# Kernel optimization log

Hardware: AMD Instinct MI355X
Metric: run time of the kernel (lower is better)

The kernel has to match this reference:

```python
import jax, jax.numpy as jnp
import numpy as np

B, S, I, H, E, V = 32, 128, 1024, 1024, 1024, 32000


def setup_inputs() -> dict:
    key = jax.random.key(0)
    ks = jax.random.split(key, 16)
    s = 0.02
    return {
        "x": jax.random.normal(ks[0], (1, B, I), jnp.float32),
        "encoder_outputs": jax.random.normal(ks[1], (S, B, E), jnp.float32),
        "hidden": jax.random.normal(ks[2], (1, B, H), jnp.float32),
        # GRU params (torch layout: gates r, z, n stacked)
        "W_ih": jax.random.normal(ks[3], (3 * H, I), jnp.float32) * s,
        "W_hh": jax.random.normal(ks[4], (3 * H, H), jnp.float32) * s,
        "b_ih": jnp.zeros((3 * H,), jnp.float32),
        "b_hh": jnp.zeros((3 * H,), jnp.float32),
        # attn: Linear(hidden + enc_hidden -> hidden)
        "W_attn": jax.random.normal(ks[5], (H, H + E), jnp.float32) * s,
        "b_attn": jnp.zeros((H,), jnp.float32),
        # attn_combine: Linear(input + enc_hidden -> input)
        "W_comb": jax.random.normal(ks[6], (I, I + E), jnp.float32) * s,
        "b_comb": jnp.zeros((I,), jnp.float32),
        # out: Linear(hidden -> vocab)
        "W_out": jax.random.normal(ks[7], (V, H), jnp.float32) * s,
        "b_out": jnp.zeros((V,), jnp.float32),
    }


def reference(x, encoder_outputs, hidden,
              W_ih, W_hh, b_ih, b_hh,
              W_attn, b_attn, W_comb, b_comb, W_out, b_out):
    Hd = hidden.shape[-1]
    x0, h0 = x[0], hidden[0]                     # [B,I], [B,H]
    # --- single GRU step (torch gate order r, z, n) ---
    xg = x0 @ W_ih.T + b_ih                      # [B,3H]
    hg = h0 @ W_hh.T + b_hh                      # [B,3H]
    r = jax.nn.sigmoid(xg[:, :Hd] + hg[:, :Hd])
    z = jax.nn.sigmoid(xg[:, Hd:2 * Hd] + hg[:, Hd:2 * Hd])
    n = jnp.tanh(xg[:, 2 * Hd:] + r * hg[:, 2 * Hd:])
    dec = (1.0 - z) * n + z * h0                 # [B,H] decoder_output
    # --- batched Bahdanau-style score: dec_b . attn([dec_b; enc_sb]) ---
    Sn = encoder_outputs.shape[0]
    dec_rep = jnp.broadcast_to(dec[None], (Sn,) + dec.shape)      # [S,B,H]
    cat = jnp.concatenate([dec_rep, encoder_outputs], axis=-1)    # [S,B,H+E]
    proj = jnp.einsum('sbc,hc->sbh', cat, W_attn) + b_attn        # [S,B,H]
    scores = jnp.einsum('bh,sbh->bs', dec, proj)                  # [B,S]
    attn_weights = jax.nn.softmax(scores, axis=-1)                # [B,S]
    context = jnp.einsum('bs,sbe->be', attn_weights, encoder_outputs)  # [B,E]
    # --- combine input + context, project to vocab, log-softmax ---
    comb = jnp.concatenate([x0, context], axis=-1) @ W_comb.T + b_comb  # [B,I]
    output = jax.nn.log_softmax(comb @ W_out.T + b_out, axis=-1)        # [B,V]
    return output, attn_weights
```

## Files before the change

### kernel.cpp

```cpp
#include <hip/hip_runtime.h>
#include <hip/hip_bf16.h>
#include <math.h>

#define BDIM 32
#define HD   1024
#define SD   128
#define VD   32000

typedef __attribute__((ext_vector_type(8))) short short8;
typedef __attribute__((ext_vector_type(4))) float floatx4;

__device__ __forceinline__ short f2bf(float f) {
    unsigned u = __builtin_bit_cast(unsigned, f);
    u += 0x7FFFu + ((u >> 16) & 1u);
    return (short)(u >> 16);
}
__device__ __forceinline__ float bf2f(short h) {
    unsigned u = ((unsigned)(unsigned short)h) << 16;
    return __builtin_bit_cast(float, u);
}
__device__ __forceinline__ unsigned pack2(float a, float b) {
    unsigned ua = __builtin_bit_cast(unsigned, a) + 0x8000u;
    unsigned ub = __builtin_bit_cast(unsigned, b) + 0x8000u;
    return (ub & 0xffff0000u) | (ua >> 16);
}

__device__ __forceinline__ int swz_idx(int b, int k) {
    int t = k >> 5, q = (k & 31) >> 3, j = k & 7;
    int mt = b >> 4, i = b & 15;
    return ((((t * 2 + mt) * 64) + q * 16 + i) << 3) + j;
}

#define MFMA(a, b, c) __builtin_amdgcn_mfma_f32_16x16x32_bf16(a, b, c, 0, 0, 0)

__global__ __launch_bounds__(256) void prep_swz(
    const float* __restrict__ x0, const float* __restrict__ h0,
    short* __restrict__ x0h, short* __restrict__ x0l,
    short* __restrict__ h0h, short* __restrict__ h0l)
{
    int idx = blockIdx.x * 256 + threadIdx.x;
    if (idx < 32768) {
        int b = idx >> 10, k = idx & 1023;
        float xv = x0[idx]; short hh = f2bf(xv);
        int d = swz_idx(b, k);
        x0h[d] = hh; x0l[d] = f2bf(xv - bf2f(hh));
    } else {
        idx -= 32768;
        int b = idx >> 10, k = idx & 1023;
        float xv = h0[idx]; short hh = f2bf(xv);
        int d = swz_idx(b, k);
        h0h[d] = hh; h0l[d] = f2bf(xv - bf2f(hh));
    }
}

template<int KCHUNK>
__device__ __forceinline__ void gemm_gates_body(
    const short* __restrict__ bhi, const short* __restrict__ blo,
    const float* __restrict__ W, float* __restrict__ out, int N, int K, int k0)
{
    int tid = threadIdx.x;
    int w = tid >> 6, l = tid & 63;
    int i = l & 15, q = l >> 4;
    int n0 = blockIdx.x * 64 + w * 16;
    const float* wrow = W + (size_t)(n0 + i) * K + q * 8;
    const short8* bph = (const short8*)bhi + l;
    const short8* bpl = (const short8*)blo + l;

    floatx4 acc0 = {0.f, 0.f, 0.f, 0.f};
    floatx4 acc1 = {0.f, 0.f, 0.f, 0.f};

#pragma unroll 2
    for (int kk = k0; kk < k0 + KCHUNK; kk += 32) {
        float4 w0 = *(const float4*)(wrow + kk);
        float4 w1 = *(const float4*)(wrow + kk + 4);
        float wf[8] = {w0.x, w0.y, w0.z, w0.w, w1.x, w1.y, w1.z, w1.w};
        short8 ahi, alo;
#pragma unroll
        for (int j = 0; j < 8; ++j) {
            short hh = f2bf(wf[j]);
            ahi[j] = hh;
            alo[j] = f2bf(wf[j] - bf2f(hh));
        }
        int t2 = (kk >> 5) * 2;
        short8 b0 = bph[(size_t)t2 * 64];
        short8 b1 = bph[(size_t)(t2 + 1) * 64];
        short8 l0 = bpl[(size_t)t2 * 64];
        short8 l1 = bpl[(size_t)(t2 + 1) * 64];
        acc0 = MFMA(ahi, b0, acc0);
        acc1 = MFMA(ahi, b1, acc1);
        acc0 = MFMA(ahi, l0, acc0);
        acc1 = MFMA(ahi, l1, acc1);
        acc0 = MFMA(alo, b0, acc0);
        acc1 = MFMA(alo, b1, acc1);
    }

    __shared__ float lds[4][32][17];
#pragma unroll
    for (int r = 0; r < 4; ++r) {
        lds[w][i][q * 4 + r]      = acc0[r];
        lds[w][i + 16][q * 4 + r] = acc1[r];
    }
    __syncthreads();
    int b = l >> 1, hf = l & 1;
    size_t obase = (size_t)b * N + n0 + hf * 8;
#pragma unroll
    for (int t = 0; t < 8; ++t) atomicAdd(out + obase + t, lds[w][b][hf * 8 + t]);
}

__global__ __launch_bounds__(256) void gemm_gates(
    const short* __restrict__ x0h, const short* __restrict__ x0l,
    const short* __restrict__ h0h, const short* __restrict__ h0l,
    const float* __restrict__ W_ih, const float* __restrict__ W_hh,
    float* __restrict__ xg, float* __restrict__ hg)
{
    if (blockIdx.z == 0)
        gemm_gates_body<512>(x0h, x0l, W_ih, xg, 3072, 1024, blockIdx.y * 512);
    else
        gemm_gates_body<512>(h0h, h0l, W_hh, hg, 3072, 1024, blockIdx.y * 512);
}

__global__ __launch_bounds__(256) void gru_gate(
    const float* __restrict__ xg, const float* __restrict__ hg,
    const float* __restrict__ h0,
    const float* __restrict__ b_ih, const float* __restrict__ b_hh,
    short* __restrict__ dh, short* __restrict__ dl)
{
    int idx = blockIdx.x * 256 + threadIdx.x;
    int b = idx >> 10, h = idx & 1023;
    const float* xp = xg + (size_t)b * 3072 + h;
    const float* hp = hg + (size_t)b * 3072 + h;
    float r = 1.f / (1.f + __expf(-(xp[0] + b_ih[h] + hp[0] + b_hh[h])));
    float z = 1.f / (1.f + __expf(-(xp[1024] + b_ih[1024 + h] +
                                    hp[1024] + b_hh[1024 + h])));
    float n = tanhf(xp[2048] + b_ih[2048 + h] + r * (hp[2048] + b_hh[2048 + h]));
    float dec = (1.f - z) * n + z * h0[idx];
    short hh = f2bf(dec);
    int d = swz_idx(b, h);
    dh[d] = hh; dl[d] = f2bf(dec - bf2f(hh));
}

__global__ __launch_bounds__(256) void gemm_attn2(
    const short* __restrict__ dhi, const short* __restrict__ dlo,
    const float* __restrict__ Wa, float* __restrict__ v)
{
    int tid = threadIdx.x, w = tid >> 6, l = tid & 63;
    int i = l & 15, q = l >> 4;
    int e0 = blockIdx.x * 64;
    int k0 = blockIdx.y * 128;
    __shared__ float lds[32][65];

    const short8* ah = (const short8*)dhi;
    const short8* al = (const short8*)dlo;
    short8 Ah[4][2], Al[4][2];
#pragma unroll
    for (int t = 0; t < 4; ++t)
#pragma unroll
        for (int mt = 0; mt < 2; ++mt) {
            size_t idx = (size_t)((((k0 >> 5) + t) * 2 + mt) * 64) + l;
            Ah[t][mt] = ah[idx]; Al[t][mt] = al[idx];
        }

    floatx4 acc[2] = {{0.f,0.f,0.f,0.f},{0.f,0.f,0.f,0.f}};
    int sr = tid >> 3;
    int sc_ = (tid & 7) * 8;
#pragma unroll
    for (int t = 0; t < 4; ++t) {
        const float* src = Wa + (size_t)(k0 + t * 32 + sr) * 2048 + 1024 + e0 + sc_;
        float4 s0 = *(const float4*)src;
        float4 s1 = *(const float4*)(src + 4);
        __syncthreads();
        *(float4*)&lds[sr][sc_]     = s0;
        *(float4*)&lds[sr][sc_ + 4] = s1;
        __syncthreads();
        short8 Bh, Bl;
#pragma unroll
        for (int j = 0; j < 8; ++j) {
            float f = lds[q * 8 + j][w * 16 + i];
            unsigned u = __builtin_bit_cast(unsigned, f);
            float hif = __builtin_bit_cast(float, u & 0xffff0000u);
            Bh[j] = (short)(u >> 16);
            float lo = f - hif;
            Bl[j] = (short)(__builtin_bit_cast(unsigned, lo) >> 16);
        }
        acc[0] = MFMA(Ah[t][0], Bh, acc[0]);
        acc[1] = MFMA(Ah[t][1], Bh, acc[1]);
        acc[0] = MFMA(Ah[t][0], Bl, acc[0]);
        acc[1] = MFMA(Ah[t][1], Bl, acc[1]);
        acc[0] = MFMA(Al[t][0], Bh, acc[0]);
        acc[1] = MFMA(Al[t][1], Bh, acc[1]);
    }
#pragma unroll
    for (int mt = 0; mt < 2; ++mt)
#pragma unroll
        for (int r = 0; r < 4; ++r)
            atomicAdd(v + (size_t)(mt * 16 + q * 4 + r) * 1024 + e0 + w * 16 + i,
                      acc[mt][r]);
}

__global__ __launch_bounds__(256) void scores_ctx(
    const float* __restrict__ v, const float* __restrict__ enc,
    float* __restrict__ num, float* __restrict__ den, float* __restrict__ es)
{
    int b = blockIdx.y, tid = threadIdx.x;
    int s0 = blockIdx.x * 8;
    int w = tid >> 6, l = tid & 63;
    float4 vv = *((const float4*)(v + (size_t)b * 1024) + tid);
    float4 e8[8];
    float part[8];
#pragma unroll
    for (int s = 0; s < 8; ++s) {
        float4 e4 = *((const float4*)(enc + ((size_t)(s0 + s) * BDIM + b) * 1024) + tid);
        e8[s] = e4;
        part[s] = e4.x * vv.x + e4.y * vv.y + e4.z * vv.z + e4.w * vv.w;
    }
    __shared__ float red[4][8];
    __shared__ float esl[8];
#pragma unroll
    for (int s = 0; s < 8; ++s) {
        float p = part[s];
        for (int o = 32; o; o >>= 1) p += __shfl_down(p, o);
        if (l == 0) red[w][s] = p;
    }
    __syncthreads();
    if (tid < 8) {
        float sc = red[0][tid] + red[1][tid] + red[2][tid] + red[3][tid];
        float e = __expf(sc);
        esl[tid] = e;
        es[b * SD + s0 + tid] = e;
    }
    __syncthreads();
    if (tid == 0) {
        float ds = 0.f;
#pragma unroll
        for (int s = 0; s < 8; ++s) ds += esl[s];
        atomicAdd(den + b, ds);
    }
    float n0 = 0.f, n1 = 0.f, n2 = 0.f, n3 = 0.f;
#pragma unroll
    for (int s = 0; s < 8; ++s) {
        float e = esl[s];
        n0 += e * e8[s].x; n1 += e * e8[s].y;
        n2 += e * e8[s].z; n3 += e * e8[s].w;
    }
    float* np = num + (size_t)b * 1024 + tid * 4;
    atomicAdd(np, n0); atomicAdd(np + 1, n1);
    atomicAdd(np + 2, n2); atomicAdd(np + 3, n3);
}

__global__ __launch_bounds__(256) void gemm_comb2(
    const float* __restrict__ x0, const float* __restrict__ num,
    const float* __restrict__ den, const float* __restrict__ es,
    const float* __restrict__ W_comb, float* __restrict__ comb,
    float* __restrict__ aw_out)
{
    int tid = threadIdx.x;
    int w = tid >> 6, l = tid & 63;
    int i = l & 15, q = l >> 4;
    int n0 = blockIdx.x * 64 + w * 16;
    int k0 = blockIdx.y * 256;
    __shared__ short cfrag[8192];

    if (blockIdx.x == 0) {
        int base = blockIdx.y * 512 + tid * 2;
#pragma unroll
        for (int j = 0; j < 2; ++j) {
            int idx = base + j;
            aw_out[idx] = es[idx] / den[idx >> 7];
        }
    }
    for (int ii = tid; ii < 8192; ii += 256) {
        int b = ii >> 8, kl = ii & 255;
        int k = k0 + kl;
        float xv = (k < 1024) ? x0[(b << 10) + k]
                              : num[(b << 10) + (k & 1023)] / den[b];
        cfrag[swz_idx(b, kl)] = f2bf(xv);
    }
    __syncthreads();

    const float* wrow = W_comb + (size_t)(n0 + i) * 2048 + k0 + q * 8;
    const short8* bp = (const short8*)cfrag + l;
    floatx4 acc0 = {0.f, 0.f, 0.f, 0.f};
    floatx4 acc1 = {0.f, 0.f, 0.f, 0.f};
#pragma unroll 2
    for (int kl = 0; kl < 256; kl += 32) {
        float4 w0 = *(const float4*)(wrow + kl);
        float4 w1 = *(const float4*)(wrow + kl + 4);
        union { unsigned u[4]; short8 s; } pk;
        pk.u[0] = pack2(w0.x, w0.y);
        pk.u[1] = pack2(w0.z, w0.w);
        pk.u[2] = pack2(w1.x, w1.y);
        pk.u[3] = pack2(w1.z, w1.w);
        int t2 = (kl >> 5) * 2;
        short8 b0 = bp[t2 * 64];
        short8 b1 = bp[(t2 + 1) * 64];
        acc0 = MFMA(pk.s, b0, acc0);
        acc1 = MFMA(pk.s, b1, acc1);
    }
    __shared__ float lds[4][32][17];
#pragma unroll
    for (int r = 0; r < 4; ++r) {
        lds[w][i][q * 4 + r]      = acc0[r];
        lds[w][i + 16][q * 4 + r] = acc1[r];
    }
    __syncthreads();
    int b = l >> 1, hf = l & 1;
    size_t obase = (size_t)b * 1024 + n0 + hf * 8;
#pragma unroll
    for (int t = 0; t < 8; ++t) atomicAdd(comb + obase + t, lds[w][b][hf * 8 + t]);
}

__global__ __launch_bounds__(256) void gemm_out2(
    const float* __restrict__ comb, const float* __restrict__ b_comb,
    const float* __restrict__ W, const float* __restrict__ bias,
    float* __restrict__ out, float* __restrict__ sexp)
{
    int tid = threadIdx.x, w = tid >> 6, l = tid & 63;
    int i = l & 15, q = l >> 4;
    int n0 = blockIdx.x * 64 + w * 16;
    __shared__ short cfrag[32768];
    __shared__ float lds[4][32][17];
    __shared__ float bsum[32];
    if (tid < 32) bsum[tid] = 0.f;
    for (int ii = tid; ii < 32768; ii += 256) {
        int b = ii >> 10, k = ii & 1023;
        cfrag[swz_idx(b, k)] = f2bf(comb[ii] + b_comb[k]);
    }
    __syncthreads();

    const float* wrow = W + (size_t)(n0 + i) * 1024 + q * 8;
    const short8* bp = (const short8*)cfrag + l;
    floatx4 acc0 = {0.f, 0.f, 0.f, 0.f};
    floatx4 acc1 = {0.f, 0.f, 0.f, 0.f};
#pragma unroll 4
    for (int kk = 0; kk < 1024; kk += 32) {
        float4 w0 = *(const float4*)(wrow + kk);
        float4 w1 = *(const float4*)(wrow + kk + 4);
        union { unsigned u[4]; short8 s; } pk;
        pk.u[0] = pack2(w0.x, w0.y);
        pk.u[1] = pack2(w0.z, w0.w);
        pk.u[2] = pack2(w1.x, w1.y);
        pk.u[3] = pack2(w1.z, w1.w);
        int t2 = (kk >> 5) * 2;
        short8 b0 = bp[t2 * 64];
        short8 b1 = bp[(t2 + 1) * 64];
        acc0 = MFMA(pk.s, b0, acc0);
        acc1 = MFMA(pk.s, b1, acc1);
    }
#pragma unroll
    for (int r = 0; r < 4; ++r) {
        lds[w][i][q * 4 + r]      = acc0[r];
        lds[w][i + 16][q * 4 + r] = acc1[r];
    }
    __syncthreads();
    int b = l >> 1, hf = l & 1;
    float vo[8];
#pragma unroll
    for (int t = 0; t < 8; ++t) vo[t] = lds[w][b][hf * 8 + t];
    const float4* bp4 = (const float4*)(bias + n0 + hf * 8);
    float4 bb0 = bp4[0], bb1 = bp4[1];
    vo[0] += bb0.x; vo[1] += bb0.y; vo[2] += bb0.z; vo[3] += bb0.w;
    vo[4] += bb1.x; vo[5] += bb1.y; vo[6] += bb1.z; vo[7] += bb1.w;
    float esum = 0.f;
#pragma unroll
    for (int t = 0; t < 8; ++t) esum += __expf(vo[t]);
    atomicAdd(&bsum[b], esum);
    float4 o0 = {vo[0], vo[1], vo[2], vo[3]};
    float4 o1 = {vo[4], vo[5], vo[6], vo[7]};
    float4* op = (float4*)(out + (size_t)b * VD + n0 + hf * 8);
    op[0] = o0; op[1] = o1;
    __syncthreads();
    if (tid < 32) atomicAdd(sexp + tid, bsum[tid]);
}

__global__ __launch_bounds__(256) void final_k(
    float* __restrict__ out, const float* __restrict__ sexp)
{
    int b = blockIdx.y;
    int vv = blockIdx.x * 256 + threadIdx.x;
    size_t o = (size_t)b * VD + vv;
    out[o] -= logf(sexp[b]);
}

extern "C" void kernel_launch(void* const* d_in, const int* in_sizes, int n_in,
                              void* d_out, int out_size, void* d_ws, size_t ws_size,
                              hipStream_t stream) {
    const float* x      = (const float*)d_in[0];
    const float* enc    = (const float*)d_in[1];
    const float* hid    = (const float*)d_in[2];
    const float* W_ih   = (const float*)d_in[3];
    const float* W_hh   = (const float*)d_in[4];
    const float* b_ih   = (const float*)d_in[5];
    const float* b_hh   = (const float*)d_in[6];
    const float* W_attn = (const float*)d_in[7];
    const float* W_comb = (const float*)d_in[9];
    const float* b_comb = (const float*)d_in[10];
    const float* W_out  = (const float*)d_in[11];
    const float* b_out  = (const float*)d_in[12];
    float* out = (float*)d_out;

    float* wsf  = (float*)d_ws;
    float* xg   = wsf;
    float* hg   = xg + 98304;
    float* v    = hg + 98304;
    float* num  = v + 32768;
    float* den  = num + 32768;
    float* sexp = den + 32;
    float* comb = sexp + 32;
    size_t zcount = 98304u * 2 + 32768u * 3 + 64;
    float* es   = comb + 32768;
    short* x0h  = (short*)(es + 4096);
    short* x0l  = x0h + 32768;
    short* h0h  = x0l + 32768;
    short* h0l  = h0h + 32768;
    short* dh   = h0l + 32768;
    short* dl   = dh + 32768;

    hipMemsetAsync(wsf, 0, zcount * sizeof(float), stream);
    prep_swz<<<256, 256, 0, stream>>>(x, hid, x0h, x0l, h0h, h0l);
    gemm_gates<<<dim3(48, 2, 2), 256, 0, stream>>>(
        x0h, x0l, h0h, h0l, W_ih, W_hh, xg, hg);
    gru_gate<<<128, 256, 0, stream>>>(xg, hg, hid, b_ih, b_hh, dh, dl);
    gemm_attn2<<<dim3(16, 8), 256, 0, stream>>>(dh, dl, W_attn, v);
    scores_ctx<<<dim3(16, 32), 256, 0, stream>>>(v, enc, num, den, es);
    gemm_comb2<<<dim3(16, 8), 256, 0, stream>>>(
        x, num, den, es, W_comb, comb, out + 1024000);
    gemm_out2<<<500, 256, 0, stream>>>(comb, b_comb, W_out, b_out, out, sexp);
    final_k<<<dim3(125, 32), 256, 0, stream>>>(out, sexp);
}
```

Measured before the change: 347.7 us.

## Fuse all decoder stages into one persistent kernel with grid barriers

Replaces the chain of eight kernel launches plus a large memset with a single persistent kernel of 512 blocks. Stages are separated by atomic-counter grid barriers, and zeroing of the workspace moves inside the kernel. The separate swizzle prep pass is dropped: the gate and combine GEMMs now read and split the activations directly. The output GEMM gets register double-buffered weight loads and one wave per 16-column tile. This removes launch gaps and intermediate traffic, but relies on all 512 blocks being co-resident (launch_bounds 256,2) and adds grid-barrier spin cost.

Result: slower. 655.2 us (+88.4%).

```diff
diff --git a/kernel.cpp b/kernel.cpp
--- a/kernel.cpp
+++ b/kernel.cpp
@@ -2,10 +2,7 @@
 #include <hip/hip_bf16.h>
 #include <math.h>
 
-#define BDIM 32
-#define HD   1024
-#define SD   128
-#define VD   32000
+#define VD 32000
 
 typedef __attribute__((ext_vector_type(8))) short short8;
 typedef __attribute__((ext_vector_type(4))) float floatx4;
@@ -24,361 +21,356 @@
     unsigned ub = __builtin_bit_cast(unsigned, b) + 0x8000u;
     return (ub & 0xffff0000u) | (ua >> 16);
 }
-
-__device__ __forceinline__ int swz_idx(int b, int k) {
-    int t = k >> 5, q = (k & 31) >> 3, j = k & 7;
-    int mt = b >> 4, i = b & 15;
-    return ((((t * 2 + mt) * 64) + q * 16 + i) << 3) + j;
+__device__ __forceinline__ void split8(const float4 u0, const float4 u1,
+                                       short8* hi, short8* lo) {
+    float f[8] = {u0.x, u0.y, u0.z, u0.w, u1.x, u1.y, u1.z, u1.w};
+#pragma unroll
+    for (int j = 0; j < 8; ++j) {
+        short h = f2bf(f[j]);
+        (*hi)[j] = h;
+        (*lo)[j] = f2bf(f[j] - bf2f(h));
+    }
+}
+__device__ __forceinline__ short8 pack8(const float4 u0, const float4 u1) {
+    union { unsigned u[4]; short8 s; } pk;
+    pk.u[0] = pack2(u0.x, u0.y); pk.u[1] = pack2(u0.z, u0.w);
+    pk.u[2] = pack2(u1.x, u1.y); pk.u[3] = pack2(u1.z, u1.w);
+    return pk.s;
 }
 
 #define MFMA(a, b, c) __builtin_amdgcn_mfma_f32_16x16x32_bf16(a, b, c, 0, 0, 0)
 
-__global__ __launch_bounds__(256) void prep_swz(
-    const float* __restrict__ x0, const float* __restrict__ h0,
-    short* __restrict__ x0h, short* __restrict__ x0l,
-    short* __restrict__ h0h, short* __restrict__ h0l)
+__device__ __forceinline__ void gbar(unsigned* bar, int ph, unsigned nb) {
+    __syncthreads();
+    if (threadIdx.x == 0) {
+        __threadfence();
+        __atomic_fetch_add(bar + ph, 1u, __ATOMIC_RELAXED);
+        while (__atomic_load_n(bar + ph, __ATOMIC_RELAXED) < nb)
+            __builtin_amdgcn_s_sleep(2);
+        __threadfence();
+    }
+    __syncthreads();
+}
+
+
+__global__ __launch_bounds__(256, 2) void mega(
+    const float* __restrict__ x0, const float* __restrict__ enc,
+    const float* __restrict__ h0,
+    const float* __restrict__ W_ih, const float* __restrict__ W_hh,
+    const float* __restrict__ b_ih, const float* __restrict__ b_hh,
+    const float* __restrict__ W_attn, const float* __restrict__ W_comb,
+    const float* __restrict__ b_comb, const float* __restrict__ W_out,
+    const float* __restrict__ b_out, float* __restrict__ out,
+    float* __restrict__ ws)
 {
-    int idx = blockIdx.x * 256 + threadIdx.x;
-    if (idx < 32768) {
-        int b = idx >> 10, k = idx & 1023;
-        float xv = x0[idx]; short hh = f2bf(xv);
-        int d = swz_idx(b, k);
-        x0h[d] = hh; x0l[d] = f2bf(xv - bf2f(hh));
-    } else {
-        idx -= 32768;
-        int b = idx >> 10, k = idx & 1023;
-        float xv = h0[idx]; short hh = f2bf(xv);
-        int d = swz_idx(b, k);
-        h0h[d] = hh; h0l[d] = f2bf(xv - bf2f(hh));
-    }
-}
-
-template<int KCHUNK>
-__device__ __forceinline__ void gemm_gates_body(
-    const short* __restrict__ bhi, const short* __restrict__ blo,
-    const float* __restrict__ W, float* __restrict__ out, int N, int K, int k0)
-{
-    int tid = threadIdx.x;
-    int w = tid >> 6, l = tid & 63;
-    int i = l & 15, q = l >> 4;
-    int n0 = blockIdx.x * 64 + w * 16;
-    const float* wrow = W + (size_t)(n0 + i) * K + q * 8;
-    const short8* bph = (const short8*)bhi + l;
-    const short8* bpl = (const short8*)blo + l;
-
-    floatx4 acc0 = {0.f, 0.f, 0.f, 0.f};
-    floatx4 acc1 = {0.f, 0.f, 0.f, 0.f};
-
-#pragma unroll 2
-    for (int kk = k0; kk < k0 + KCHUNK; kk += 32) {
-        float4 w0 = *(const float4*)(wrow + kk);
-        float4 w1 = *(const float4*)(wrow + kk + 4);
-        float wf[8] = {w0.x, w0.y, w0.z, w0.w, w1.x, w1.y, w1.z, w1.w};
-        short8 ahi, alo;
-#pragma unroll
-        for (int j = 0; j < 8; ++j) {
-            short hh = f2bf(wf[j]);
-            ahi[j] = hh;
-            alo[j] = f2bf(wf[j] - bf2f(hh));
-        }
-        int t2 = (kk >> 5) * 2;
-        short8 b0 = bph[(size_t)t2 * 64];
-        short8 b1 = bph[(size_t)(t2 + 1) * 64];
-        short8 l0 = bpl[(size_t)t2 * 64];
-        short8 l1 = bpl[(size_t)(t2 + 1) * 64];
-        acc0 = MFMA(ahi, b0, acc0);
-        acc1 = MFMA(ahi, b1, acc1);
-        acc0 = MFMA(ahi, l0, acc0);
-        acc1 = MFMA(ahi, l1, acc1);
-        acc0 = MFMA(alo, b0, acc0);
-        acc1 = MFMA(alo, b1, acc1);
-    }
-
-    __shared__ float lds[4][32][17];
-#pragma unroll
-    for (int r = 0; r < 4; ++r) {
-        lds[w][i][q * 4 + r]      = acc0[r];
-        lds[w][i + 16][q * 4 + r] = acc1[r];
-    }
-    __syncthreads();
-    int b = l >> 1, hf = l & 1;
-    size_t obase = (size_t)b * N + n0 + hf * 8;
-#pragma unroll
-    for (int t = 0; t < 8; ++t) atomicAdd(out + obase + t, lds[w][b][hf * 8 + t]);
-}
-
-__global__ __launch_bounds__(256) void gemm_gates(
-    const short* __restrict__ x0h, const short* __restrict__ x0l,
-    const short* __restrict__ h0h, const short* __restrict__ h0l,
-    const float* __restrict__ W_ih, const float* __restrict__ W_hh,
-    float* __restrict__ xg, float* __restrict__ hg)
-{
-    if (blockIdx.z == 0)
-        gemm_gates_body<512>(x0h, x0l, W_ih, xg, 3072, 1024, blockIdx.y * 512);
-    else
-        gemm_gates_body<512>(h0h, h0l, W_hh, hg, 3072, 1024, blockIdx.y * 512);
-}
-
-__global__ __launch_bounds__(256) void gru_gate(
-    const float* __restrict__ xg, const float* __restrict__ hg,
-    const float* __restrict__ h0,
-    const float* __restrict__ b_ih, const float* __restrict__ b_hh,
-    short* __restrict__ dh, short* __restrict__ dl)
-{
-    int idx = blockIdx.x * 256 + threadIdx.x;
-    int b = idx >> 10, h = idx & 1023;
-    const float* xp = xg + (size_t)b * 3072 + h;
-    const float* hp = hg + (size_t)b * 3072 + h;
-    float r = 1.f / (1.f + __expf(-(xp[0] + b_ih[h] + hp[0] + b_hh[h])));
-    float z = 1.f / (1.f + __expf(-(xp[1024] + b_ih[1024 + h] +
-                                    hp[1024] + b_hh[1024 + h])));
-    float n = tanhf(xp[2048] + b_ih[2048 + h] + r * (hp[2048] + b_hh[2048 + h]));
-    float dec = (1.f - z) * n + z * h0[idx];
-    short hh = f2bf(dec);
-    int d = swz_idx(b, h);
-    dh[d] = hh; dl[d] = f2bf(dec - bf2f(hh));
-}
-
-__global__ __launch_bounds__(256) void gemm_attn2(
-    const short* __restrict__ dhi, const short* __restrict__ dlo,
-    const float* __restrict__ Wa, float* __restrict__ v)
-{
-    int tid = threadIdx.x, w = tid >> 6, l = tid & 63;
-    int i = l & 15, q = l >> 4;
-    int e0 = blockIdx.x * 64;
-    int k0 = blockIdx.y * 128;
-    __shared__ float lds[32][65];
-
-    const short8* ah = (const short8*)dhi;
-    const short8* al = (const short8*)dlo;
-    short8 Ah[4][2], Al[4][2];
-#pragma unroll
-    for (int t = 0; t < 4; ++t)
-#pragma unroll
-        for (int mt = 0; mt < 2; ++mt) {
-            size_t idx = (size_t)((((k0 >> 5) + t) * 2 + mt) * 64) + l;
-            Ah[t][mt] = ah[idx]; Al[t][mt] = al[idx];
-        }
-
-    floatx4 acc[2] = {{0.f,0.f,0.f,0.f},{0.f,0.f,0.f,0.f}};
-    int sr = tid >> 3;
-    int sc_ = (tid & 7) * 8;
-#pragma unroll
-    for (int t = 0; t < 4; ++t) {
-        const float* src = Wa + (size_t)(k0 + t * 32 + sr) * 2048 + 1024 + e0 + sc_;
-        float4 s0 = *(const float4*)src;
-        float4 s1 = *(const float4*)(src + 4);
-        __syncthreads();
-        *(float4*)&lds[sr][sc_]     = s0;
-        *(float4*)&lds[sr][sc_ + 4] = s1;
-        __syncthreads();
-        short8 Bh, Bl;
-#pragma unroll
-        for (int j = 0; j < 8; ++j) {
-            float f = lds[q * 8 + j][w * 16 + i];
-            unsigned u = __builtin_bit_cast(unsigned, f);
-            float hif = __builtin_bit_cast(float, u & 0xffff0000u);
-            Bh[j] = (short)(u >> 16);
-            float lo = f - hif;
-            Bl[j] = (short)(__builtin_bit_cast(unsigned, lo) >> 16);
-        }
-        acc[0] = MFMA(Ah[t][0], Bh, acc[0]);
-        acc[1] = MFMA(Ah[t][1], Bh, acc[1]);
-        acc[0] = MFMA(Ah[t][0], Bl, acc[0]);
-        acc[1] = MFMA(Ah[t][1], Bl, acc[1]);
-        acc[0] = MFMA(Al[t][0], Bh, acc[0]);
-        acc[1] = MFMA(Al[t][1], Bh, acc[1]);
-    }
-#pragma unroll
-    for (int mt = 0; mt < 2; ++mt)
-#pragma unroll
-        for (int r = 0; r < 4; ++r)
-            atomicAdd(v + (size_t)(mt * 16 + q * 4 + r) * 1024 + e0 + w * 16 + i,
-                      acc[mt][r]);
-}
-
-__global__ __launch_bounds__(256) void scores_ctx(
-    const float* __restrict__ v, const float* __restrict__ enc,
-    float* __restrict__ num, float* __restrict__ den, float* __restrict__ es)
-{
-    int b = blockIdx.y, tid = threadIdx.x;
-    int s0 = blockIdx.x * 8;
-    int w = tid >> 6, l = tid & 63;
-    float4 vv = *((const float4*)(v + (size_t)b * 1024) + tid);
-    float4 e8[8];
-    float part[8];
-#pragma unroll
-    for (int s = 0; s < 8; ++s) {
-        float4 e4 = *((const float4*)(enc + ((size_t)(s0 + s) * BDIM + b) * 1024) + tid);
-        e8[s] = e4;
-        part[s] = e4.x * vv.x + e4.y * vv.y + e4.z * vv.z + e4.w * vv.w;
-    }
+    const int gid = blockIdx.x, tid = threadIdx.x;
+    const unsigned NB = gridDim.x;
+    const int gt = gid * 256 + tid;
+    const int wv = tid >> 6, l = tid & 63;
+    const int i = l & 15, q = l >> 4;
+
+    unsigned* bar = (unsigned*)ws;
+    float* wsf   = ws + 16;
+    float* xg    = wsf;
+    float* hg    = xg + 98304;
+    float* v     = hg + 98304;
+    float* num   = v + 32768;
+    float* den   = num + 32768;
+    float* sexp  = den + 32;
+    float* comb  = sexp + 32;
+    float* es    = comb + 32768;
+    float* dec   = es + 4096;
+    short* combh = (short*)(dec + 32768);
+
+    __shared__ float stage[32][65];
+    __shared__ float eplds[4][32][17];
+    __shared__ float bsum[32];
     __shared__ float red[4][8];
     __shared__ float esl[8];
-#pragma unroll
-    for (int s = 0; s < 8; ++s) {
-        float p = part[s];
-        for (int o = 32; o; o >>= 1) p += __shfl_down(p, o);
-        if (l == 0) red[w][s] = p;
-    }
-    __syncthreads();
-    if (tid < 8) {
-        float sc = red[0][tid] + red[1][tid] + red[2][tid] + red[3][tid];
-        float e = __expf(sc);
-        esl[tid] = e;
-        es[b * SD + s0 + tid] = e;
-    }
-    __syncthreads();
-    if (tid == 0) {
-        float ds = 0.f;
-#pragma unroll
-        for (int s = 0; s < 8; ++s) ds += esl[s];
-        atomicAdd(den + b, ds);
-    }
-    float n0 = 0.f, n1 = 0.f, n2 = 0.f, n3 = 0.f;
-#pragma unroll
-    for (int s = 0; s < 8; ++s) {
-        float e = esl[s];
-        n0 += e * e8[s].x; n1 += e * e8[s].y;
-        n2 += e * e8[s].z; n3 += e * e8[s].w;
-    }
-    float* np = num + (size_t)b * 1024 + tid * 4;
-    atomicAdd(np, n0); atomicAdd(np + 1, n1);
-    atomicAdd(np + 2, n2); atomicAdd(np + 3, n3);
-}
-
-__global__ __launch_bounds__(256) void gemm_comb2(
-    const float* __restrict__ x0, const float* __restrict__ num,
-    const float* __restrict__ den, const float* __restrict__ es,
-    const float* __restrict__ W_comb, float* __restrict__ comb,
-    float* __restrict__ aw_out)
-{
-    int tid = threadIdx.x;
-    int w = tid >> 6, l = tid & 63;
-    int i = l & 15, q = l >> 4;
-    int n0 = blockIdx.x * 64 + w * 16;
-    int k0 = blockIdx.y * 256;
-    __shared__ short cfrag[8192];
-
-    if (blockIdx.x == 0) {
-        int base = blockIdx.y * 512 + tid * 2;
-#pragma unroll
-        for (int j = 0; j < 2; ++j) {
-            int idx = base + j;
-            aw_out[idx] = es[idx] / den[idx >> 7];
-        }
-    }
-    for (int ii = tid; ii < 8192; ii += 256) {
-        int b = ii >> 8, kl = ii & 255;
-        int k = k0 + kl;
-        float xv = (k < 1024) ? x0[(b << 10) + k]
-                              : num[(b << 10) + (k & 1023)] / den[b];
-        cfrag[swz_idx(b, kl)] = f2bf(xv);
-    }
-    __syncthreads();
-
-    const float* wrow = W_comb + (size_t)(n0 + i) * 2048 + k0 + q * 8;
-    const short8* bp = (const short8*)cfrag + l;
-    floatx4 acc0 = {0.f, 0.f, 0.f, 0.f};
-    floatx4 acc1 = {0.f, 0.f, 0.f, 0.f};
+
+    {
+        float4* z4 = (float4*)wsf;
+        if (gt < 73744) z4[gt] = make_float4(0.f, 0.f, 0.f, 0.f);
+    }
+    gbar(bar, 0, NB);
+
+    if (gid < 384) {
+        const int z = gid & 1, kc = (gid >> 1) & 3, nt = gid >> 3;
+        const int n0 = nt * 64 + wv * 16, k0 = kc * 256;
+        const float* W   = z ? W_hh : W_ih;
+        const float* act = z ? h0   : x0;
+        float*       o   = z ? hg   : xg;
+        const float* wrow = W + (size_t)(n0 + i) * 1024 + q * 8;
+        const float* a0 = act + (size_t)i * 1024 + q * 8;
+        const float* a1 = act + (size_t)(16 + i) * 1024 + q * 8;
+        floatx4 acc0 = {0.f,0.f,0.f,0.f}, acc1 = {0.f,0.f,0.f,0.f};
 #pragma unroll 2
-    for (int kl = 0; kl < 256; kl += 32) {
-        float4 w0 = *(const float4*)(wrow + kl);
-        float4 w1 = *(const float4*)(wrow + kl + 4);
-        union { unsigned u[4]; short8 s; } pk;
-        pk.u[0] = pack2(w0.x, w0.y);
-        pk.u[1] = pack2(w0.z, w0.w);
-        pk.u[2] = pack2(w1.x, w1.y);
-        pk.u[3] = pack2(w1.z, w1.w);
-        int t2 = (kl >> 5) * 2;
-        short8 b0 = bp[t2 * 64];
-        short8 b1 = bp[(t2 + 1) * 64];
-        acc0 = MFMA(pk.s, b0, acc0);
-        acc1 = MFMA(pk.s, b1, acc1);
-    }
-    __shared__ float lds[4][32][17];
-#pragma unroll
-    for (int r = 0; r < 4; ++r) {
-        lds[w][i][q * 4 + r]      = acc0[r];
-        lds[w][i + 16][q * 4 + r] = acc1[r];
-    }
-    __syncthreads();
-    int b = l >> 1, hf = l & 1;
-    size_t obase = (size_t)b * 1024 + n0 + hf * 8;
-#pragma unroll
-    for (int t = 0; t < 8; ++t) atomicAdd(comb + obase + t, lds[w][b][hf * 8 + t]);
-}
-
-__global__ __launch_bounds__(256) void gemm_out2(
-    const float* __restrict__ comb, const float* __restrict__ b_comb,
-    const float* __restrict__ W, const float* __restrict__ bias,
-    float* __restrict__ out, float* __restrict__ sexp)
-{
-    int tid = threadIdx.x, w = tid >> 6, l = tid & 63;
-    int i = l & 15, q = l >> 4;
-    int n0 = blockIdx.x * 64 + w * 16;
-    __shared__ short cfrag[32768];
-    __shared__ float lds[4][32][17];
-    __shared__ float bsum[32];
-    if (tid < 32) bsum[tid] = 0.f;
-    for (int ii = tid; ii < 32768; ii += 256) {
-        int b = ii >> 10, k = ii & 1023;
-        cfrag[swz_idx(b, k)] = f2bf(comb[ii] + b_comb[k]);
-    }
-    __syncthreads();
-
-    const float* wrow = W + (size_t)(n0 + i) * 1024 + q * 8;
-    const short8* bp = (const short8*)cfrag + l;
-    floatx4 acc0 = {0.f, 0.f, 0.f, 0.f};
-    floatx4 acc1 = {0.f, 0.f, 0.f, 0.f};
-#pragma unroll 4
-    for (int kk = 0; kk < 1024; kk += 32) {
-        float4 w0 = *(const float4*)(wrow + kk);
-        float4 w1 = *(const float4*)(wrow + kk + 4);
-        union { unsigned u[4]; short8 s; } pk;
-        pk.u[0] = pack2(w0.x, w0.y);
-        pk.u[1] = pack2(w0.z, w0.w);
-        pk.u[2] = pack2(w1.x, w1.y);
-        pk.u[3] = pack2(w1.z, w1.w);
-        int t2 = (kk >> 5) * 2;
-        short8 b0 = bp[t2 * 64];
-        short8 b1 = bp[(t2 + 1) * 64];
-        acc0 = MFMA(pk.s, b0, acc0);
-        acc1 = MFMA(pk.s, b1, acc1);
-    }
-#pragma unroll
-    for (int r = 0; r < 4; ++r) {
-        lds[w][i][q * 4 + r]      = acc0[r];
-        lds[w][i + 16][q * 4 + r] = acc1[r];
-    }
-    __syncthreads();
-    int b = l >> 1, hf = l & 1;
-    float vo[8];
-#pragma unroll
-    for (int t = 0; t < 8; ++t) vo[t] = lds[w][b][hf * 8 + t];
-    const float4* bp4 = (const float4*)(bias + n0 + hf * 8);
-    float4 bb0 = bp4[0], bb1 = bp4[1];
-    vo[0] += bb0.x; vo[1] += bb0.y; vo[2] += bb0.z; vo[3] += bb0.w;
-    vo[4] += bb1.x; vo[5] += bb1.y; vo[6] += bb1.z; vo[7] += bb1.w;
-    float esum = 0.f;
-#pragma unroll
-    for (int t = 0; t < 8; ++t) esum += __expf(vo[t]);
-    atomicAdd(&bsum[b], esum);
-    float4 o0 = {vo[0], vo[1], vo[2], vo[3]};
-    float4 o1 = {vo[4], vo[5], vo[6], vo[7]};
-    float4* op = (float4*)(out + (size_t)b * VD + n0 + hf * 8);
-    op[0] = o0; op[1] = o1;
-    __syncthreads();
-    if (tid < 32) atomicAdd(sexp + tid, bsum[tid]);
-}
-
-__global__ __launch_bounds__(256) void final_k(
-    float* __restrict__ out, const float* __restrict__ sexp)
-{
-    int b = blockIdx.y;
-    int vv = blockIdx.x * 256 + threadIdx.x;
-    size_t o = (size_t)b * VD + vv;
-    out[o] -= logf(sexp[b]);
+        for (int kk = k0; kk < k0 + 256; kk += 32) {
+            float4 w0 = *(const float4*)(wrow + kk);
+            float4 w1 = *(const float4*)(wrow + kk + 4);
+            float4 p0 = *(const float4*)(a0 + kk);
+            float4 p1 = *(const float4*)(a0 + kk + 4);
+            float4 r0 = *(const float4*)(a1 + kk);
+            float4 r1 = *(const float4*)(a1 + kk + 4);
+            short8 ah, al, b0h, b0l, b1h, b1l;
+            split8(w0, w1, &ah, &al);
+            split8(p0, p1, &b0h, &b0l);
+            split8(r0, r1, &b1h, &b1l);
+            acc0 = MFMA(ah, b0h, acc0);
+            acc0 = MFMA(ah, b0l, acc0);
+            acc0 = MFMA(al, b0h, acc0);
+            acc1 = MFMA(ah, b1h, acc1);
+            acc1 = MFMA(ah, b1l, acc1);
+            acc1 = MFMA(al, b1h, acc1);
+        }
+#pragma unroll
+        for (int r = 0; r < 4; ++r) {
+            eplds[wv][i][q * 4 + r]      = acc0[r];
+            eplds[wv][i + 16][q * 4 + r] = acc1[r];
+        }
+        int b = l >> 1, hf = l & 1;
+        size_t obase = (size_t)b * 3072 + n0 + hf * 8;
+#pragma unroll
+        for (int t = 0; t < 8; ++t)
+            atomicAdd(o + obase + t, eplds[wv][b][hf * 8 + t]);
+    }
+    gbar(bar, 1, NB);
+
+    if (gt < 32768) {
+        int b = gt >> 10, h = gt & 1023;
+        const float* xp = xg + (size_t)b * 3072 + h;
+        const float* hp = hg + (size_t)b * 3072 + h;
+        float r = 1.f / (1.f + __expf(-(xp[0] + b_ih[h] + hp[0] + b_hh[h])));
+        float z = 1.f / (1.f + __expf(-(xp[1024] + b_ih[1024 + h] +
+                                        hp[1024] + b_hh[1024 + h])));
+        float n = tanhf(xp[2048] + b_ih[2048 + h] +
+                        r * (hp[2048] + b_hh[2048 + h]));
+        dec[gt] = (1.f - z) * n + z * h0[gt];
+    }
+    gbar(bar, 2, NB);
+
+    if (gid < 256) {
+        const int et = gid & 15, kc = gid >> 4;
+        const int e0 = et * 64, k0 = kc * 64;
+        const int sr = tid >> 3, sc = (tid & 7) * 8;
+        floatx4 acc0 = {0.f,0.f,0.f,0.f}, acc1 = {0.f,0.f,0.f,0.f};
+#pragma unroll
+        for (int t = 0; t < 2; ++t) {
+            int kb = k0 + t * 32;
+            const float* src = W_attn + (size_t)(kb + sr) * 2048 + 1024 + e0 + sc;
+            float4 s0 = *(const float4*)src;
+            float4 s1 = *(const float4*)(src + 4);
+            __syncthreads();
+            *(float4*)&stage[sr][sc]     = s0;
+            *(float4*)&stage[sr][sc + 4] = s1;
+            __syncthreads();
+            short8 Ah0, Al0, Ah1, Al1, Bh, Bl;
+            {
+                const float* dp = dec + (size_t)i * 1024 + kb + q * 8;
+                split8(*(const float4*)dp, *(const float4*)(dp + 4), &Ah0, &Al0);
+                const float* dp1 = dec + (size_t)(16 + i) * 1024 + kb + q * 8;
+                split8(*(const float4*)dp1, *(const float4*)(dp1 + 4), &Ah1, &Al1);
+            }
+#pragma unroll
+            for (int j = 0; j < 8; ++j) {
+                float f = stage[q * 8 + j][wv * 16 + i];
+                unsigned u = __builtin_bit_cast(unsigned, f);
+                float hif = __builtin_bit_cast(float, u & 0xffff0000u);
+                Bh[j] = (short)(u >> 16);
+                Bl[j] = (short)(__builtin_bit_cast(unsigned, f - hif) >> 16);
+            }
+            acc0 = MFMA(Ah0, Bh, acc0);
+            acc0 = MFMA(Ah0, Bl, acc0);
+            acc0 = MFMA(Al0, Bh, acc0);
+            acc1 = MFMA(Ah1, Bh, acc1);
+            acc1 = MFMA(Ah1, Bl, acc1);
+            acc1 = MFMA(Al1, Bh, acc1);
+        }
+#pragma unroll
+        for (int r = 0; r < 4; ++r) {
+            atomicAdd(v + (size_t)(q * 4 + r) * 1024 + e0 + wv * 16 + i, acc0[r]);
+            atomicAdd(v + (size_t)(16 + q * 4 + r) * 1024 + e0 + wv * 16 + i, acc1[r]);
+        }
+    }
+    gbar(bar, 3, NB);
+
+    {
+        int b = gid & 31, s0 = (gid >> 5) * 8;
+        float4 vv = *((const float4*)(v + (size_t)b * 1024) + tid);
+        float4 e8[8];
+        float part[8];
+#pragma unroll
+        for (int s = 0; s < 8; ++s) {
+            float4 e4 = *((const float4*)(enc + ((size_t)(s0 + s) * 32 + b) * 1024) + tid);
+            e8[s] = e4;
+            part[s] = e4.x * vv.x + e4.y * vv.y + e4.z * vv.z + e4.w * vv.w;
+        }
+#pragma unroll
+        for (int s = 0; s < 8; ++s) {
+            float p = part[s];
+            for (int o = 32; o; o >>= 1) p += __shfl_down(p, o);
+            if (l == 0) red[wv][s] = p;
+        }
+        __syncthreads();
+        if (tid < 8) {
+            float sc_ = red[0][tid] + red[1][tid] + red[2][tid] + red[3][tid];
+            float e = __expf(sc_);
+            esl[tid] = e;
+            es[b * 128 + s0 + tid] = e;
+        }
+        __syncthreads();
+        if (tid == 0) {
+            float ds = 0.f;
+#pragma unroll
+            for (int s = 0; s < 8; ++s) ds += esl[s];
+            atomicAdd(den + b, ds);
+        }
+        float n0 = 0.f, n1 = 0.f, n2 = 0.f, n3 = 0.f;
+#pragma unroll
+        for (int s = 0; s < 8; ++s) {
+            float e = esl[s];
+            n0 += e * e8[s].x; n1 += e * e8[s].y;
+            n2 += e * e8[s].z; n3 += e * e8[s].w;
+        }
+        float* np = num + (size_t)b * 1024 + tid * 4;
+        atomicAdd(np, n0); atomicAdd(np + 1, n1);
+        atomicAdd(np + 2, n2); atomicAdd(np + 3, n3);
+    }
+    gbar(bar, 4, NB);
+
+    if (gid < 128) {
+        const int nt = gid & 15, kc = gid >> 4;
+        const int n0 = nt * 64 + wv * 16, k0 = kc * 256;
+        const bool isnum = kc >= 4;
+        const float* base = isnum ? num : x0;
+        const int kb = isnum ? k0 - 1024 : k0;
+        float rd0 = 1.f, rd1 = 1.f;
+        if (isnum) { rd0 = 1.f / den[i]; rd1 = 1.f / den[16 + i]; }
+        const float* wrow = W_comb + (size_t)(n0 + i) * 2048 + k0 + q * 8;
+        const float* a0 = base + (size_t)i * 1024 + kb + q * 8;
+        const float* a1 = base + (size_t)(16 + i) * 1024 + kb + q * 8;
+        floatx4 acc0 = {0.f,0.f,0.f,0.f}, acc1 = {0.f,0.f,0.f,0.f};
+#pragma unroll 2
+        for (int kk = 0; kk < 256; kk += 32) {
+            float4 w0 = *(const float4*)(wrow + kk);
+            float4 w1 = *(const float4*)(wrow + kk + 4);
+            float4 p0 = *(const float4*)(a0 + kk);
+            float4 p1 = *(const float4*)(a0 + kk + 4);
+            float4 r0 = *(const float4*)(a1 + kk);
+            float4 r1 = *(const float4*)(a1 + kk + 4);
+            short8 af = pack8(w0, w1);
+            short8 b0f, b1f;
+            float c0[8] = {p0.x,p0.y,p0.z,p0.w,p1.x,p1.y,p1.z,p1.w};
+            float c1[8] = {r0.x,r0.y,r0.z,r0.w,r1.x,r1.y,r1.z,r1.w};
+#pragma unroll
+            for (int j = 0; j < 8; ++j) {
+                b0f[j] = f2bf(c0[j] * rd0);
+                b1f[j] = f2bf(c1[j] * rd1);
+            }
+            acc0 = MFMA(af, b0f, acc0);
+            acc1 = MFMA(af, b1f, acc1);
+        }
+#pragma unroll
+        for (int r = 0; r < 4; ++r) {
+            eplds[wv][i][q * 4 + r]      = acc0[r];
+            eplds[wv][i + 16][q * 4 + r] = acc1[r];
+        }
+        int b = l >> 1, hf = l & 1;
+        size_t obase = (size_t)b * 1024 + n0 + hf * 8;
+#pragma unroll
+        for (int t = 0; t < 8; ++t)
+            atomicAdd(comb + obase + t, eplds[wv][b][hf * 8 + t]);
+        if (nt == 0) {
+            float* aw = out + 1024000;
+            int bi = kc * 512 + tid * 2;
+#pragma unroll
+            for (int j = 0; j < 2; ++j) {
+                int idx = bi + j;
+                aw[idx] = es[idx] / den[idx >> 7];
+            }
+        }
+    }
+    gbar(bar, 5, NB);
+
+    if (gt < 32768) {
+        int d = gt;
+        int j = d & 7, ii = (d >> 3) & 15, qq = (d >> 7) & 3, T = d >> 9;
+        int b = (T & 1) * 16 + ii;
+        int k = (T >> 1) * 32 + qq * 8 + j;
+        combh[d] = f2bf(comb[b * 1024 + k] + b_comb[k]);
+    }
+    gbar(bar, 6, NB);
+
+    {
+        if (tid < 32) bsum[tid] = 0.f;
+        __syncthreads();
+        const int gw = gid * 4 + wv;
+        if (gw < 2000) {
+            const int n0 = gw * 16;
+            const float* wrow = W_out + (size_t)(n0 + i) * 1024 + q * 8;
+            const short8* bp = (const short8*)combh + l;
+            float4 wa = *(const float4*)(wrow);
+            float4 wb = *(const float4*)(wrow + 4);
+            short8 f0 = bp[0], f1 = bp[64];
+            floatx4 acc0 = {0.f,0.f,0.f,0.f}, acc1 = {0.f,0.f,0.f,0.f};
+#pragma unroll
+            for (int kk = 0; kk < 992; kk += 32) {
+                float4 na = *(const float4*)(wrow + kk + 32);
+                float4 nb = *(const float4*)(wrow + kk + 36);
+                int t2 = ((kk >> 5) + 1) * 2;
+                short8 g0 = bp[t2 * 64];
+                short8 g1 = bp[t2 * 64 + 64];
+                short8 af = pack8(wa, wb);
+                acc0 = MFMA(af, f0, acc0);
+                acc1 = MFMA(af, f1, acc1);
+                wa = na; wb = nb; f0 = g0; f1 = g1;
+            }
+            {
+                short8 af = pack8(wa, wb);
+                acc0 = MFMA(af, f0, acc0);
+                acc1 = MFMA(af, f1, acc1);
+            }
+#pragma unroll
+            for (int r = 0; r < 4; ++r) {
+                eplds[wv][i][q * 4 + r]      = acc0[r];
+                eplds[wv][i + 16][q * 4 + r] = acc1[r];
+            }
+            int b = l >> 1, hf = l & 1;
+            float vo[8];
+#pragma unroll
+            for (int t = 0; t < 8; ++t) vo[t] = eplds[wv][b][hf * 8 + t];
+            const float4* bo = (const float4*)(b_out + n0 + hf * 8);
+            float4 bb0 = bo[0], bb1 = bo[1];
+            vo[0] += bb0.x; vo[1] += bb0.y; vo[2] += bb0.z; vo[3] += bb0.w;
+            vo[4] += bb1.x; vo[5] += bb1.y; vo[6] += bb1.z; vo[7] += bb1.w;
+            float esum = 0.f;
+#pragma unroll
+            for (int t = 0; t < 8; ++t) esum += __expf(vo[t]);
+            atomicAdd(&bsum[b], esum);
+            float4 o0 = {vo[0], vo[1], vo[2], vo[3]};
+            float4 o1 = {vo[4], vo[5], vo[6], vo[7]};
+            float4* op = (float4*)(out + (size_t)b * VD + n0 + hf * 8);
+            op[0] = o0; op[1] = o1;
+        }
+        __syncthreads();
+        if (tid < 32) atomicAdd(sexp + tid, bsum[tid]);
+    }
+    gbar(bar, 7, NB);
+
+    {
+        float4* o4 = (float4*)out;
+#pragma unroll
+        for (int rep = 0; rep < 2; ++rep) {
+            int idx4 = gt + rep * 131072;
+            if (idx4 < 256000) {
+                int b = idx4 / 8000;
+                float ls = logf(sexp[b]);
+                float4 t = o4[idx4];
+                t.x -= ls; t.y -= ls; t.z -= ls; t.w -= ls;
+                o4[idx4] = t;
+            }
+        }
+    }
 }
 
 extern "C" void kernel_launch(void* const* d_in, const int* in_sizes, int n_in,
@@ -397,33 +389,10 @@
     const float* W_out  = (const float*)d_in[11];
     const float* b_out  = (const float*)d_in[12];
     float* out = (float*)d_out;
-
-    float* wsf  = (float*)d_ws;
-    float* xg   = wsf;
-    float* hg   = xg + 98304;
-    float* v    = hg + 98304;
-    float* num  = v + 32768;
-    float* den  = num + 32768;
-    float* sexp = den + 32;
-    float* comb = sexp + 32;
-    size_t zcount = 98304u * 2 + 32768u * 3 + 64;
-    float* es   = comb + 32768;
-    short* x0h  = (short*)(es + 4096);
-    short* x0l  = x0h + 32768;
-    short* h0h  = x0l + 32768;
-    short* h0l  = h0h + 32768;
-    short* dh   = h0l + 32768;
-    short* dl   = dh + 32768;
-
-    hipMemsetAsync(wsf, 0, zcount * sizeof(float), stream);
-    prep_swz<<<256, 256, 0, stream>>>(x, hid, x0h, x0l, h0h, h0l);
-    gemm_gates<<<dim3(48, 2, 2), 256, 0, stream>>>(
-        x0h, x0l, h0h, h0l, W_ih, W_hh, xg, hg);
-    gru_gate<<<128, 256, 0, stream>>>(xg, hg, hid, b_ih, b_hh, dh, dl);
-    gemm_attn2<<<dim3(16, 8), 256, 0, stream>>>(dh, dl, W_attn, v);
-    scores_ctx<<<dim3(16, 32), 256, 0, stream>>>(v, enc, num, den, es);
-    gemm_comb2<<<dim3(16, 8), 256, 0, stream>>>(
-        x, num, den, es, W_comb, comb, out + 1024000);
-    gemm_out2<<<500, 256, 0, stream>>>(comb, b_comb, W_out, b_out, out, sexp);
-    final_k<<<dim3(125, 32), 256, 0, stream>>>(out, sexp);
-}
+    float* wsf = (float*)d_ws;
+
+    hipMemsetAsync(d_ws, 0, 64, stream);
+    mega<<<512, 256, 0, stream>>>(x, enc, hid, W_ih, W_hh, b_ih, b_hh,
+                                  W_attn, W_comb, b_comb, W_out, b_out,
+                                  out, wsf);
+}
```
